# Kernel tuning notes

Hardware: AMD Instinct MI355X
Metric: run time of the kernel (lower is better)

## Reference

```python
import jax, jax.numpy as jnp
import numpy as np

V = 50257  # vocab
D = 256    # embedding size
H = 256    # hidden size
E = 64     # pre-allocated entity slots (replaces dynamic torch.cat growth)
T = 2048   # sequence length


def setup_inputs() -> dict:
    key = jax.random.key(0)
    ks = jax.random.split(key, 16)

    def n(k, shape, s=0.02):
        return (jax.random.normal(k, shape) * s).astype(jnp.float32)

    r_emb = n(ks[0], (2, H))
    # Equation 7: entity slot init = r_emb[1] + sigma*noise, L2-normalized per row
    noise = jax.random.normal(ks[1], (E, H)).astype(jnp.float32)
    u = r_emb[1][None, :] + 0.01 * noise
    entities_init = u / jnp.linalg.norm(u, axis=-1, keepdims=True)

    return dict(
        tokens=jax.random.randint(ks[2], (T,), 0, V),
        entity_ids=jax.random.randint(ks[3], (T,), 0, E),
        emb=n(ks[4], (V, D)),
        W_ih=n(ks[5], (4 * H, D)),
        W_hh=n(ks[6], (4 * H, H)),
        b_ih=jnp.zeros((4 * H,), jnp.float32),
        b_hh=jnp.zeros((4 * H,), jnp.float32),
        out_W=n(ks[7], (V, H)),
        out_b=jnp.zeros((V,), jnp.float32),
        r_emb=r_emb,
        Wr_W=n(ks[8], (1, H, H)), Wr_b=jnp.zeros((1,), jnp.float32),
        Wlen_W=n(ks[9], (25, 2 * H)), Wlen_b=jnp.zeros((25,), jnp.float32),
        Went_W=n(ks[10], (1, H, H)), Went_b=jnp.zeros((1,), jnp.float32),
        wdist_W=n(ks[11], (1, 1)), wdist_b=jnp.zeros((1,), jnp.float32),
        Wdelta_W=n(ks[12], (1, H, H)), Wdelta_b=jnp.zeros((1,), jnp.float32),
        We_W=n(ks[13], (H, H)), We_b=jnp.zeros((H,), jnp.float32),
        entities_init=entities_init,
        dist_init=jnp.zeros((E, 1), jnp.float32),
    )


def _forward(tokens, entity_ids, emb, W_ih, W_hh, b_ih, b_hh, out_W, out_b,
             r_emb, Wr_W, Wr_b, Wlen_W, Wlen_b, Went_W, Went_b,
             wdist_W, wdist_b, Wdelta_W, Wdelta_b, We_W, We_b,
             entities_init, dist_init):
    def step(carry, inp):
        h, c, ents, dists, t = carry
        tok, eid = inp
        # single-step LSTM (torch gate order i, f, g, o)
        x = emb[tok]
        gates = W_ih @ x + b_ih + W_hh @ h + b_hh
        i_, f_, g_, o_ = jnp.split(gates, 4)
        c = jax.nn.sigmoid(f_) * c + jax.nn.sigmoid(i_) * jnp.tanh(g_)
        h = jax.nn.sigmoid(o_) * jnp.tanh(c)
        # Equation 3: pred_r = Bilinear(r_emb, h)  -> [2]
        pred_r = r_emb @ (Wr_W[0] @ h) + Wr_b[0]
        # Equation 4: entity scores with distance feature  -> [E]
        dist = dists[:, 0] - t                                    # dist_features - t
        h_aug = h[None, :] + (dist[:, None] * wdist_W[0, 0] + wdist_b[0])  # [E,H]
        pred_e = jnp.sum((ents @ Went_W[0]) * h_aug, axis=-1) + Went_b[0]
        # current entity read (gather)
        e_cur = ents[eid]
        # Equation 5: length head  -> [25]
        pred_l = Wlen_W @ jnp.concatenate([h, e_cur]) + Wlen_b
        # next-word logits  -> [V]
        pred_x = out_W @ (h + We_W @ e_cur + We_b) + out_b
        # Equation 8: entity update + scatter
        delta = jax.nn.sigmoid(e_cur @ (Wdelta_W[0] @ h) + Wdelta_b[0])
        u = delta * e_cur + (1.0 - delta) * h
        u = u / jnp.linalg.norm(u)
        ents = ents.at[eid].set(u)
        dists = dists.at[eid, 0].set(t)
        out = jnp.concatenate([pred_r, pred_e, pred_l, pred_x])  # [2+E+25+V]
        return (h, c, ents, dists, t + 1.0), out

    carry0 = (jnp.zeros((H,), jnp.float32), jnp.zeros((H,), jnp.float32),
              entities_init, dist_init, jnp.float32(0.0))
    _, outs = jax.lax.scan(step, carry0, (tokens, entity_ids))
    return outs  # [T, 2+E+25+V]


def reference(tokens, entity_ids, emb, W_ih, W_hh, b_ih, b_hh, out_W, out_b,
              r_emb, Wr_W, Wr_b, Wlen_W, Wlen_b, Went_W, Went_b,
              wdist_W, wdist_b, Wdelta_W, Wdelta_b, We_W, We_b,
              entities_init, dist_init):
    return _forward(tokens, entity_ids, emb, W_ih, W_hh, b_ih, b_hh, out_W, out_b,
                    r_emb, Wr_W, Wr_b, Wlen_W, Wlen_b, Went_W, Went_b,
                    wdist_W, wdist_b, Wdelta_W, Wdelta_b, We_W, We_b,
                    entities_init, dist_init)
```

## Files before the change

kernel.cpp:

```cpp
#include <hip/hip_runtime.h>
#include <cstdint>
#include <cstddef>

#define V_  50257
#define H_  256
#define E_  64
#define T_  2048
#define G4_ 1024
#define OSTRIDE 50348
#define CMROWS 820
#define PSTR 832
#define NGRP 16
#define RPB 52
#define NPREB 32
#define WSTR 257

typedef __attribute__((ext_vector_type(2))) _Float16 half2v;
typedef __attribute__((ext_vector_type(8))) short short8v;
typedef __attribute__((ext_vector_type(4))) float floatx4;

__device__ __forceinline__ float fdot2u(unsigned a, unsigned b, float acc){
  return __builtin_amdgcn_fdot2(__builtin_bit_cast(half2v, a),
                                __builtin_bit_cast(half2v, b), acc, false);
}
__device__ __forceinline__ unsigned packh2(float a, float b){
  half2v h; h.x = (_Float16)a; h.y = (_Float16)b;
  return __builtin_bit_cast(unsigned, h);
}
__device__ __forceinline__ unsigned short f2bf(float f){
  unsigned u = __builtin_bit_cast(unsigned, f);
  u += 0x7fffu + ((u >> 16) & 1u);
  return (unsigned short)(u >> 16);
}
__device__ __forceinline__ float sigm(float x){
  return __builtin_amdgcn_rcpf(1.0f + __expf(-x));
}
__device__ __forceinline__ float tanh_f(float x){
  float e = __expf(2.0f * x);
  return (e - 1.0f) * __builtin_amdgcn_rcpf(e + 1.0f);
}
__device__ __forceinline__ float dot4(uint4 w, uint4 h, float acc){
  acc = fdot2u(w.x, h.x, acc); acc = fdot2u(w.y, h.y, acc);
  acc = fdot2u(w.z, h.z, acc); acc = fdot2u(w.w, h.w, acc);
  return acc;
}

__device__ __forceinline__ int ldi_rlx(int* p){
  return __hip_atomic_load(p, __ATOMIC_RELAXED, __HIP_MEMORY_SCOPE_AGENT);
}
__device__ __forceinline__ float ldf_rlx(const float* p){
  return __hip_atomic_load(p, __ATOMIC_RELAXED, __HIP_MEMORY_SCOPE_AGENT);
}
__device__ __forceinline__ void stf_rlx(float* p, float v){
  __hip_atomic_store(p, v, __ATOMIC_RELAXED, __HIP_MEMORY_SCOPE_AGENT);
}
__device__ __forceinline__ void flag_add(int* p){
  (void)__hip_atomic_fetch_add(p, 1, __ATOMIC_RELAXED, __HIP_MEMORY_SCOPE_AGENT);
}

__global__ void k_prep(const float* __restrict__ out_W, const float* __restrict__ W_ih,
                       const float* __restrict__ W_hh,
                       unsigned short* __restrict__ OWB, float* __restrict__ WT,
                       unsigned* __restrict__ WP){
  const long n0 = (long)V_ * H_;
  const long n1 = (long)G4_ * H_;
  const long n2 = 32l * G4_;
  const long total = n0 + n1 + n2;
  for (long id = (long)blockIdx.x * blockDim.x + threadIdx.x; id < total;
       id += (long)gridDim.x * blockDim.x){
    if (id < n0){
      OWB[id] = f2bf(out_W[id]);
    } else if (id < n0 + n1){
      long i = id - n0;
      int r = (int)(i & 1023), k = (int)(i >> 10);
      WT[i] = W_ih[r * H_ + k];
    } else {
      long i = id - n0 - n1;
      int t = (int)(i & 1023), j4 = (int)(i >> 10);
      int r0 = t >> 2, s = t & 3;
      #pragma unroll
      for (int d = 0; d < 4; ++d){
        int j = j4 * 4 + d;
        int ri = j >> 5, c = j & 31;
        int grow = ri * H_ + r0;
        int k0 = s * 64 + c * 2;
        WP[(j4 * 1024 + t) * 4 + d] = packh2(W_hh[grow * H_ + k0],
                                             W_hh[grow * H_ + k0 + 1]);
      }
    }
  }
}

__global__ void k_cm(const float* __restrict__ Wdelta, const float* __restrict__ Went,
                     const float* __restrict__ We, const float* __restrict__ r_emb,
                     const float* __restrict__ Wr, const float* __restrict__ Wlen,
                     float* __restrict__ CMR){
  const int total = CMROWS * H_;
  for (int id = blockIdx.x * blockDim.x + threadIdx.x; id < total;
       id += gridDim.x * blockDim.x){
    int r = id >> 8, k = id & 255;
    float v;
    if (r < 256)      v = Wdelta[r * H_ + k];
    else if (r < 512) v = Went[k * H_ + (r - 256)];
    else if (r < 768) v = We[(r - 512) * H_ + k];
    else if (r < 770){
      int i = r - 768; float acc = 0.f;
      for (int m = 0; m < H_; ++m) acc += r_emb[i * H_ + m] * Wr[m * H_ + k];
      v = acc;
    }
    else if (r < 795) v = Wlen[(r - 770) * 2 * H_ + k];
    else              v = Wlen[(r - 795) * 2 * H_ + H_ + k];
    CMR[r * H_ + k] = v;
  }
}

__global__ void k_init(const float* __restrict__ E0, const float* __restrict__ Went,
                       const float* __restrict__ We, const float* __restrict__ Wlen,
                       float* __restrict__ GI, float* __restrict__ MST,
                       float* __restrict__ LST, float* __restrict__ ENTS){
  const int nG = E_ * H_, nM = E_ * H_, nL = E_ * 32, nC = E_ * H_;
  const int total = nG + nM + nL + nC;
  for (int id = blockIdx.x * blockDim.x + threadIdx.x; id < total;
       id += gridDim.x * blockDim.x){
    if (id < nG){
      int j = id >> 8, i = id & 255; float a = 0.f;
      for (int k = 0; k < H_; ++k) a += E0[j * H_ + k] * Went[k * H_ + i];
      GI[id] = a;
    } else if (id < nG + nM){
      int x = id - nG; int j = x >> 8, i = x & 255; float a = 0.f;
      for (int k = 0; k < H_; ++k) a += E0[j * H_ + k] * We[i * H_ + k];
      MST[x] = a;
    } else if (id < nG + nM + nL){
      int x = id - nG - nM; int j = x >> 5, i = x & 31; float a = 0.f;
      if (i < 25)
        for (int k = 0; k < H_; ++k) a += E0[j * H_ + k] * Wlen[i * 2 * H_ + H_ + k];
      LST[x] = a;
    } else {
      int x = id - nG - nM - nL;
      ENTS[x] = E0[x];
    }
  }
}

__global__ __launch_bounds__(1024) void k_a(const int* __restrict__ tokens,
                                            const float* __restrict__ emb,
                                            const float* __restrict__ WT,
                                            const float* __restrict__ b_ih,
                                            const float* __restrict__ b_hh,
                                            float* __restrict__ A4){
  __shared__ __align__(16) float xs[H_][8];
  const int t0 = blockIdx.x * 8;
  const int tid = threadIdx.x;
  for (int id = tid; id < 8 * H_; id += 1024){
    int k = id >> 3, tl = id & 7;
    xs[k][tl] = emb[(size_t)tokens[t0 + tl] * H_ + k];
  }
  __syncthreads();
  const int r = tid;
  const float base = b_ih[r] + b_hh[r];
  float acc[8];
  #pragma unroll
  for (int i = 0; i < 8; ++i) acc[i] = base;
  for (int k = 0; k < H_; ++k){
    float w = WT[k * G4_ + r];
    floatx4 x0 = *(const floatx4*)&xs[k][0];
    floatx4 x1 = *(const floatx4*)&xs[k][4];
    acc[0] += w * x0.x; acc[1] += w * x0.y; acc[2] += w * x0.z; acc[3] += w * x0.w;
    acc[4] += w * x1.x; acc[5] += w * x1.y; acc[6] += w * x1.z; acc[7] += w * x1.w;
  }
  const int r0 = r & 255, g = r >> 8;
  #pragma unroll
  for (int tl = 0; tl < 8; ++tl)
    A4[(((t0 + tl) * H_ + r0) << 2) + g] = acc[tl];
}

struct LstmS { unsigned hsh[4 * 36]; uint4 olds[7 * 512]; };
struct PreS  { float wrow[RPB * WSTR]; float hbuf[H_]; };
struct EntS  {
  unsigned Gsh[E_ * 132];
  unsigned hsh2[2][128];
  float Hld[2][H_], Dld[2][H_], Wld[2][H_], Vld[2][H_];
  float EXs[2][64];
  float Ssh[E_], DSH[E_];
  float red[8][2];
  float sc[4];
};
union PipeS { LstmS l; PreS p; EntS e; };

__global__ __launch_bounds__(512, 1) void k_pipe(
    const uint4* __restrict__ WP4, const floatx4* __restrict__ A4,
    float* Hws, const float* __restrict__ CMR, float* PRE,
    const int* __restrict__ ids, const float* __restrict__ GI,
    const float* __restrict__ dist_init, const float* __restrict__ We_b,
    const float* __restrict__ Wlen_b, const float* __restrict__ wdW,
    const float* __restrict__ wdB, const float* __restrict__ WdeltaB,
    const float* __restrict__ WentB, const float* __restrict__ WrB,
    float* __restrict__ ENTS, float* __restrict__ MST, float* __restrict__ LST,
    unsigned short* __restrict__ Zb, float* __restrict__ out,
    int* prog_h, int* pre_done)
{
  __shared__ PipeS sm;
  const int tid = threadIdx.x;
  const int bid = blockIdx.x;

  if (bid == 0){
    unsigned* hsh = sm.l.hsh;
    uint4* olds = sm.l.olds;
    const int r0 = tid >> 1, s2 = tid & 1;
    const int tA = r0 * 4 + 2 * s2;
    const int tB = tA + 1;
    const int sA = 2 * s2;

    uint4 wA[32], wB[16];
    #pragma unroll
    for (int j4 = 0; j4 < 32; ++j4) wA[j4] = WP4[j4 * 1024 + tA];
    #pragma unroll
    for (int j4 = 0; j4 < 16; ++j4) wB[j4] = WP4[j4 * 1024 + tB];
    #pragma unroll
    for (int j4 = 24; j4 < 31; ++j4) olds[(j4 - 24) * 512 + tid] = WP4[j4 * 1024 + tB];
    if (tid < 144) hsh[tid] = 0u;

    const uint4* gsrc = &WP4[16 * 1024 + tB];
    uint4 g_cur = gsrc[0];
    float c = 0.0f;
    floatx4 a_cur = A4[r0];
    floatx4 a_nxt = a_cur;
    __syncthreads();

    for (int t = 0; t < T_; ++t){
      if (t + 1 < T_) a_nxt = A4[(t + 1) * H_ + r0];
      uint4 o_strm = gsrc[15 * 1024];
      float acc0 = a_cur.x * 0.5f, acc1 = a_cur.y * 0.5f;
      float acc2 = a_cur.z * 0.5f, acc3 = a_cur.w * 0.5f;
      #pragma unroll
      for (int cc = 0; cc < 8; ++cc){
        uint4 g_nxt = gsrc[((cc < 7) ? (cc + 1) : 0) * 1024];
        uint4 hA = *(const uint4*)&hsh[sA * 36 + cc * 4];
        uint4 hB = *(const uint4*)&hsh[sA * 36 + 36 + cc * 4];
        acc0 = dot4(wA[cc],      hA, acc0);
        acc1 = dot4(wA[8 + cc],  hA, acc1);
        acc2 = dot4(wA[16 + cc], hA, acc2);
        acc3 = dot4(wA[24 + cc], hA, acc3);
        acc0 = dot4(wB[cc],      hB, acc0);
        acc1 = dot4(wB[8 + cc],  hB, acc1);
        acc2 = dot4(g_cur,       hB, acc2);
        uint4 xo = (cc < 7) ? olds[cc * 512 + tid] : o_strm;
        acc3 = dot4(xo,          hB, acc3);
        g_cur = g_nxt;
      }
      acc0 += __shfl_xor(acc0, 1);
      acc1 += __shfl_xor(acc1, 1);
      acc2 += __shfl_xor(acc2, 1);
      acc3 += __shfl_xor(acc3, 1);
      float ci = sigm(acc0), cf = sigm(acc1), cg = tanh_f(acc2), co = sigm(acc3);
      c = cf * c + ci * cg;
      float hn = co * tanh_f(c);
      __syncthreads();
      if (s2 == 0){
        ((_Float16*)hsh)[(((r0 >> 6) * 36) + ((r0 >> 1) & 31)) * 2 + (r0 & 1)] = (_Float16)hn;
        stf_rlx(&Hws[t * H_ + r0], hn);
      }
      __syncthreads();
      if (tid == 0) flag_add(prog_h);
      a_cur = a_nxt;
    }
  } else if (bid <= NPREB){
    float* wrow = sm.p.wrow;
    float* hbuf = sm.p.hbuf;
    const int w9 = bid - 1;
    const int grp = w9 & (NGRP - 1), ph = w9 >> 4;
    const int rbase = grp * RPB;
    const int nrows = (rbase + RPB <= CMROWS) ? RPB : (CMROWS - rbase);
    for (int id = tid; id < nrows * H_; id += 512){
      int lr = id >> 8, k = id & 255;
      wrow[lr * WSTR + k] = CMR[(size_t)rbase * H_ + id];
    }
    __syncthreads();
    for (int t = ph; t < T_; t += 2){
      if (tid == 0){
        while (ldi_rlx(prog_h) < t + 1) __builtin_amdgcn_s_sleep(8);
      }
      __syncthreads();
      if (tid < H_) hbuf[tid] = ldf_rlx(&Hws[t * H_ + tid]);
      __syncthreads();
      if (tid < nrows){
        const float* wr = &wrow[tid * WSTR];
        float a = 0.f;
        #pragma unroll 8
        for (int k = 0; k < H_; ++k) a += wr[k] * hbuf[k];
        stf_rlx(&PRE[(size_t)t * PSTR + rbase + tid], a);
      }
      __syncthreads();
      if (tid == 0) flag_add(&pre_done[t]);
    }
  } else {
    EntS& E = sm.e;
    unsigned* Gsh = E.Gsh;
    auto& hsh2 = E.hsh2;
    auto& Hld = E.Hld; auto& Dld = E.Dld; auto& Wld = E.Wld; auto& Vld = E.Vld;
    auto& EXs = E.EXs;
    float* Ssh = E.Ssh; float* DSH = E.DSH;
    auto& red = E.red; float* sc = E.sc;

    for (int id = tid; id < E_ * 128; id += 512){
      int j = id >> 7, cx = id & 127;
      Gsh[j * 132 + cx] = packh2(GI[j * H_ + 2 * cx], GI[j * H_ + 2 * cx + 1]);
    }
    if (tid < E_){
      float ssum = 0.f;
      for (int k = 0; k < H_; ++k) ssum += GI[tid * H_ + k];
      Ssh[tid] = ssum;
      DSH[tid] = dist_init[tid];
    }
    const float wd = wdW[0], wdb = wdB[0], bdel = WdeltaB[0];
    const float wentb = WentB[0], wrb = WrB[0];
    int eid = ids[0];
    int eidn = ids[1];
    float e_k = 0.f, m_k = 0.f, web = 0.f;
    float l_i = 0.f, wlb = 0.f;
    if (tid == 0){
      while (ldi_rlx(&pre_done[0]) < NGRP) __builtin_amdgcn_s_sleep(2);
    }
    __syncthreads();
    if (tid < H_){
      e_k = ENTS[eid * H_ + tid];
      m_k = MST[eid * H_ + tid];
      web = We_b[tid];
      float h0 = ldf_rlx(&Hws[tid]);
      Hld[0][tid] = h0;
      ((_Float16*)&hsh2[0][0])[tid] = (_Float16)h0;
      Dld[0][tid] = ldf_rlx(&PRE[tid]);
      Wld[0][tid] = ldf_rlx(&PRE[256 + tid]);
      Vld[0][tid] = ldf_rlx(&PRE[512 + tid]);
    }
    if (tid < 25){ l_i = LST[eid * 32 + tid]; wlb = Wlen_b[tid]; }
    if (tid >= 256 && tid < 308) EXs[0][tid - 256] = ldf_rlx(&PRE[768 + (tid - 256)]);
    int dv = NGRP;
    if (T_ > 1) dv = ldi_rlx(&pre_done[1]);
    __syncthreads();

    const int jrow = tid >> 3, sl = tid & 7;
    const int wave = tid >> 6;

    for (int t = 0; t < T_; ++t){
      const int par = t & 1;
      float Hn = 0.f, Dn = 0.f, Wn = 0.f, Vn = 0.f, EXn = 0.f;
      if (t + 1 < T_){
        if (tid < 320 && dv < NGRP){
          while (ldi_rlx(&pre_done[t + 1]) < NGRP) __builtin_amdgcn_s_sleep(2);
        }
        if (tid < H_){
          Hn = ldf_rlx(&Hws[(t + 1) * H_ + tid]);
          float* p = &PRE[(size_t)(t + 1) * PSTR];
          Dn = ldf_rlx(&p[tid]); Wn = ldf_rlx(&p[256 + tid]); Vn = ldf_rlx(&p[512 + tid]);
        } else if (tid < 308){
          EXn = ldf_rlx(&PRE[(size_t)(t + 1) * PSTR + 768 + (tid - 256)]);
        }
        if (tid < 320)
          dv = (t + 2 < T_) ? ldi_rlx(&pre_done[t + 2]) : NGRP;
      }
      const int eid2 = ids[(t + 2 < T_) ? (t + 2) : (T_ - 1)];
      const bool swr = (eidn != eid);
      float e2 = 0.f, m2 = 0.f, l2 = 0.f;
      if (swr){
        if (tid < H_){ e2 = ENTS[eidn * H_ + tid]; m2 = MST[eidn * H_ + tid]; }
        if (tid < 25)  l2 = LST[eidn * 32 + tid];
      }
      float pe = 0.f;
      {
        const unsigned* gp = &Gsh[jrow * 132 + sl * 16];
        const unsigned* hp = &hsh2[par][sl * 16];
        uint4 g0 = *(const uint4*)&gp[0];
        uint4 g1 = *(const uint4*)&gp[4];
        uint4 g2 = *(const uint4*)&gp[8];
        uint4 g3 = *(const uint4*)&gp[12];
        uint4 h0 = *(const uint4*)&hp[0];
        uint4 h1 = *(const uint4*)&hp[4];
        uint4 h2 = *(const uint4*)&hp[8];
        uint4 h3 = *(const uint4*)&hp[12];
        pe = dot4(g0, h0, pe); pe = dot4(g1, h1, pe);
        pe = dot4(g2, h2, pe); pe = dot4(g3, h3, pe);
        pe += __shfl_xor(pe, 1); pe += __shfl_xor(pe, 2); pe += __shfl_xor(pe, 4);
      }
      if (sl == 0){
        float dist = DSH[jrow] - (float)t;
        out[(size_t)t * OSTRIDE + 2 + jrow] = pe + (dist * wd + wdb) * Ssh[jrow] + wentb;
      }
      if (tid < H_){
        float pd = e_k * Dld[par][tid];
        float pw = Wld[par][tid];
        #pragma unroll
        for (int m = 1; m < 64; m <<= 1){ pd += __shfl_xor(pd, m); pw += __shfl_xor(pw, m); }
        if ((tid & 63) == 0){ red[wave][0] = pd; red[wave][1] = pw; }
      }
      __syncthreads();
      if (tid == 0){
        float sd = red[0][0] + red[1][0] + red[2][0] + red[3][0];
        float swt = red[0][1] + red[1][1] + red[2][1] + red[3][1];
        sc[0] = sigm(sd + bdel);
        sc[1] = swt;
      }
      __syncthreads();
      const float del = sc[0];
      float u = 0.f;
      if (tid < H_){
        u = del * e_k + (1.0f - del) * Hld[par][tid];
        float pu = u * u;
        #pragma unroll
        for (int m = 1; m < 64; m <<= 1) pu += __shfl_xor(pu, m);
        if ((tid & 63) == 0) red[wave][0] = pu;
      }
      __syncthreads();
      if (tid == 0)
        sc[2] = __builtin_amdgcn_rsqf(red[0][0] + red[1][0] + red[2][0] + red[3][0]);
      __syncthreads();
      const float rn = sc[2];
      float un = 0.f, mn = 0.f;
      if (tid < H_){
        un = u * rn;
        ENTS[eid * H_ + tid] = un;
        mn = (del * m_k + (1.0f - del) * Vld[par][tid]) * rn;
        MST[eid * H_ + tid] = mn;
        float z = Hld[par][tid] + m_k + web;
        Zb[(size_t)t * H_ + tid] = f2bf(z);
      }
      if (tid < 128){
        unsigned gp2 = Gsh[eid * 132 + tid];
        half2v g = __builtin_bit_cast(half2v, gp2);
        float gl = (del * (float)g.x + (1.0f - del) * Wld[par][2 * tid    ]) * rn;
        float gh = (del * (float)g.y + (1.0f - del) * Wld[par][2 * tid + 1]) * rn;
        Gsh[eid * 132 + tid] = packh2(gl, gh);
      }
      float ln = 0.f;
      if (tid < 25){
        out[(size_t)t * OSTRIDE + 66 + tid] = EXs[par][2 + tid] + l_i + wlb;
        ln = (del * l_i + (1.0f - del) * EXs[par][27 + tid]) * rn;
        LST[eid * 32 + tid] = ln;
      }
      if (tid < 2) out[(size_t)t * OSTRIDE + tid] = EXs[par][tid] + wrb;
      if (tid == 0){
        Ssh[eid] = (del * Ssh[eid] + (1.0f - del) * sc[1]) * rn;
        DSH[eid] = (float)t;
      }
      if (t + 1 < T_){
        if (tid < H_){
          Hld[1 - par][tid] = Hn; Dld[1 - par][tid] = Dn;
          Wld[1 - par][tid] = Wn; Vld[1 - par][tid] = Vn;
          ((_Float16*)&hsh2[1 - par][0])[tid] = (_Float16)Hn;
        } else if (tid < 308){
          EXs[1 - par][tid - 256] = EXn;
        }
      }
      if (tid < H_){ e_k = swr ? e2 : un; m_k = swr ? m2 : mn; }
      if (tid < 25)  l_i = swr ? l2 : ln;
      eid = eidn; eidn = eid2;
      __syncthreads();
    }
  }
}

__global__ __launch_bounds__(256) void k_gemm(const unsigned short* __restrict__ OWB,
                                              const unsigned short* __restrict__ Zb,
                                              const float* __restrict__ out_b,
                                              float* __restrict__ out){
  __shared__ __align__(16) unsigned short Ash[128 * 72];
  __shared__ __align__(16) unsigned short Bsh[128 * 72];
  const int t0 = blockIdx.x * 128;
  const int v0 = blockIdx.y * 128;
  const int tid = threadIdx.x;
  const int lane = tid & 63, w = tid >> 6;
  const int mb = (w & 1) * 64, nb = (w >> 1) * 64;
  const int q = lane >> 4, fr = lane & 15;
  floatx4 acc[4][4];
  #pragma unroll
  for (int a = 0; a < 4; ++a)
    #pragma unroll
    for (int b = 0; b < 4; ++b) acc[a][b] = (floatx4){0.f, 0.f, 0.f, 0.f};
  for (int kt = 0; kt < 4; ++kt){
    if (kt) __syncthreads();
    #pragma unroll
    for (int it = 0; it < 4; ++it){
      int task = it * 256 + tid;
      int r = task >> 3, c8 = task & 7;
      int gk = kt * 64 + c8 * 8;
      uint4 av;
      if (v0 + r < V_) av = *(const uint4*)&OWB[(size_t)(v0 + r) * H_ + gk];
      else { av.x = 0; av.y = 0; av.z = 0; av.w = 0; }
      *(uint4*)&Ash[r * 72 + c8 * 8] = av;
      uint4 bv = *(const uint4*)&Zb[(size_t)(t0 + r) * H_ + gk];
      *(uint4*)&Bsh[r * 72 + c8 * 8] = bv;
    }
    __syncthreads();
    #pragma unroll
    for (int ks = 0; ks < 2; ++ks){
      short8v af[4], bf[4];
      #pragma unroll
      for (int mi = 0; mi < 4; ++mi)
        af[mi] = *(const short8v*)&Ash[(mb + mi * 16 + fr) * 72 + ks * 32 + q * 8];
      #pragma unroll
      for (int ni = 0; ni < 4; ++ni)
        bf[ni] = *(const short8v*)&Bsh[(nb + ni * 16 + fr) * 72 + ks * 32 + q * 8];
      #pragma unroll
      for (int mi = 0; mi < 4; ++mi)
        #pragma unroll
        for (int ni = 0; ni < 4; ++ni)
          acc[mi][ni] = __builtin_amdgcn_mfma_f32_16x16x32_bf16(af[mi], bf[ni],
                                                                acc[mi][ni], 0, 0, 0);
    }
  }
  #pragma unroll
  for (int mi = 0; mi < 4; ++mi){
    #pragma unroll
    for (int ni = 0; ni < 4; ++ni){
      int tt = t0 + nb + ni * 16 + fr;
      int vv = v0 + mb + mi * 16 + q * 4;
      float* op = out + (size_t)tt * OSTRIDE + 91 + vv;
      #pragma unroll
      for (int r2 = 0; r2 < 4; ++r2){
        int v = vv + r2;
        if (v < V_) op[r2] = acc[mi][ni][r2] + out_b[v];
      }
    }
  }
}

extern "C" void kernel_launch(void* const* d_in, const int* in_sizes, int n_in,
                              void* d_out, int out_size, void* d_ws, size_t ws_size,
                              hipStream_t stream){
  (void)in_sizes; (void)n_in; (void)out_size; (void)ws_size;
  const int*   tokens  = (const int*)d_in[0];
  const int*   eids    = (const int*)d_in[1];
  const float* emb     = (const float*)d_in[2];
  const float* W_ih    = (const float*)d_in[3];
  const float* W_hh    = (const float*)d_in[4];
  const float* b_ih    = (const float*)d_in[5];
  const float* b_hh    = (const float*)d_in[6];
  const float* out_W   = (const float*)d_in[7];
  const float* out_b   = (const float*)d_in[8];
  const float* r_emb   = (const float*)d_in[9];
  const float* Wr_W    = (const float*)d_in[10];
  const float* Wr_b    = (const float*)d_in[11];
  const float* Wlen_W  = (const float*)d_in[12];
  const float* Wlen_b  = (const float*)d_in[13];
  const float* Went_W  = (const float*)d_in[14];
  const float* Went_b  = (const float*)d_in[15];
  const float* wdist_W = (const float*)d_in[16];
  const float* wdist_b = (const float*)d_in[17];
  const float* Wdelta_W= (const float*)d_in[18];
  const float* Wdelta_b= (const float*)d_in[19];
  const float* We_W    = (const float*)d_in[20];
  const float* We_b    = (const float*)d_in[21];
  const float* E0      = (const float*)d_in[22];
  const float* dist0   = (const float*)d_in[23];
  float* out = (float*)d_out;

  char* ws = (char*)d_ws;
  size_t off = 0;
  auto alloc = [&](size_t bytes) -> void* {
    void* p = ws + off;
    off += (bytes + 255) & ~(size_t)255;
    return p;
  };
  float* WT    = (float*)alloc(sizeof(float) * H_ * G4_);
  float* A4    = (float*)alloc(sizeof(float) * (size_t)T_ * H_ * 4);
  unsigned* WP = (unsigned*)alloc(sizeof(unsigned) * 32 * 1024 * 4);
  float* Hws   = (float*)alloc(sizeof(float) * (size_t)T_ * H_);
  float* CMR   = (float*)alloc(sizeof(float) * CMROWS * H_);
  float* PRE   = (float*)alloc(sizeof(float) * (size_t)T_ * PSTR);
  float* ENTS  = (float*)alloc(sizeof(float) * E_ * H_);
  float* MST   = (float*)alloc(sizeof(float) * E_ * H_);
  float* LST   = (float*)alloc(sizeof(float) * E_ * 32);
  float* GI    = (float*)alloc(sizeof(float) * E_ * H_);
  unsigned short* Zb  = (unsigned short*)alloc(sizeof(short) * (size_t)T_ * H_);
  unsigned short* OWB = (unsigned short*)alloc(sizeof(short) * (size_t)V_ * H_);
  int* pre_done = (int*)alloc(sizeof(int) * (T_ + 64));
  int* prog_h   = pre_done + T_;

  hipMemsetAsync(pre_done, 0, sizeof(int) * (T_ + 64), stream);
  hipLaunchKernelGGL(k_prep, dim3(4096), dim3(256), 0, stream,
                     out_W, W_ih, W_hh, OWB, WT, WP);
  hipLaunchKernelGGL(k_cm, dim3(512), dim3(256), 0, stream,
                     Wdelta_W, Went_W, We_W, r_emb, Wr_W, Wlen_W, CMR);
  hipLaunchKernelGGL(k_init, dim3(256), dim3(256), 0, stream,
                     E0, Went_W, We_W, Wlen_W, GI, MST, LST, ENTS);
  hipLaunchKernelGGL(k_a, dim3(T_ / 8), dim3(1024), 0, stream,
                     tokens, emb, WT, b_ih, b_hh, A4);
  hipLaunchKernelGGL(k_pipe, dim3(2 + NPREB), dim3(512), 0, stream,
                     (const uint4*)WP, (const floatx4*)A4, Hws, CMR, PRE,
                     eids, GI, dist0, We_b, Wlen_b,
                     wdist_W, wdist_b, Wdelta_b, Went_b, Wr_b,
                     ENTS, MST, LST, Zb, out, prog_h, pre_done);
  hipLaunchKernelGGL(k_gemm, dim3(16, 393), dim3(256), 0, stream,
                     OWB, Zb, out_b, out);
}
```

Measured before the change: 4.444 ms.

## Fuse vocab GEMM into persistent pipeline kernel, overlapping with sequential entity recurrence

Moves the output-projection GEMM into the persistent pipeline kernel as 222 extra blocks. Each block waits on an entity-progress counter and computes 128x128 tiles as soon as the matching Zb rows are written, so the large GEMM overlaps the serial recurrence instead of running after it. The change also merges the k_cm, k_init and memset work into k_prep, and removes two barriers per step in the entity loop by having every thread do the reductions. In exchange, all blocks must be co-resident because of the spin-waits, which risks deadlock or contention with the latency-critical recurrence blocks, and half the threads in each GEMM block sit idle during the MFMA phase.

```diff
diff --git a/kernel.cpp b/kernel.cpp
--- a/kernel.cpp
+++ b/kernel.cpp
@@ -14,6 +14,9 @@
 #define RPB 52
 #define NPREB 32
 #define WSTR 257
+#define NGEMB 222
+#define NTILT 16
+#define NTILV 393
 
 typedef __attribute__((ext_vector_type(2))) _Float16 half2v;
 typedef __attribute__((ext_vector_type(8))) short short8v;
@@ -59,13 +62,23 @@
 }
 
 __global__ void k_prep(const float* __restrict__ out_W, const float* __restrict__ W_ih,
-                       const float* __restrict__ W_hh,
+                       const float* __restrict__ W_hh, const float* __restrict__ Wdelta,
+                       const float* __restrict__ Went, const float* __restrict__ We,
+                       const float* __restrict__ r_emb, const float* __restrict__ Wr,
+                       const float* __restrict__ Wlen, const float* __restrict__ E0,
                        unsigned short* __restrict__ OWB, float* __restrict__ WT,
-                       unsigned* __restrict__ WP){
+                       unsigned* __restrict__ WP, float* __restrict__ CMR,
+                       float* __restrict__ GI, float* __restrict__ MST,
+                       float* __restrict__ LST, float* __restrict__ ENTS,
+                       int* __restrict__ FLG){
   const long n0 = (long)V_ * H_;
   const long n1 = (long)G4_ * H_;
   const long n2 = 32l * G4_;
-  const long total = n0 + n1 + n2;
+  const long n3 = (long)CMROWS * H_;
+  const long nG = E_ * H_, nM = E_ * H_, nL = E_ * 32, nC = E_ * H_;
+  const long n4 = nG + nM + nL + nC;
+  const long n5 = T_ + 64;
+  const long total = n0 + n1 + n2 + n3 + n4 + n5;
   for (long id = (long)blockIdx.x * blockDim.x + threadIdx.x; id < total;
        id += (long)gridDim.x * blockDim.x){
     if (id < n0){
@@ -74,7 +87,7 @@
       long i = id - n0;
       int r = (int)(i & 1023), k = (int)(i >> 10);
       WT[i] = W_ih[r * H_ + k];
-    } else {
+    } else if (id < n0 + n1 + n2){
       long i = id - n0 - n1;
       int t = (int)(i & 1023), j4 = (int)(i >> 10);
       int r0 = t >> 2, s = t & 3;
@@ -87,57 +100,42 @@
         WP[(j4 * 1024 + t) * 4 + d] = packh2(W_hh[grow * H_ + k0],
                                              W_hh[grow * H_ + k0 + 1]);
       }
-    }
-  }
-}
-
-__global__ void k_cm(const float* __restrict__ Wdelta, const float* __restrict__ Went,
-                     const float* __restrict__ We, const float* __restrict__ r_emb,
-                     const float* __restrict__ Wr, const float* __restrict__ Wlen,
-                     float* __restrict__ CMR){
-  const int total = CMROWS * H_;
-  for (int id = blockIdx.x * blockDim.x + threadIdx.x; id < total;
-       id += gridDim.x * blockDim.x){
-    int r = id >> 8, k = id & 255;
-    float v;
-    if (r < 256)      v = Wdelta[r * H_ + k];
-    else if (r < 512) v = Went[k * H_ + (r - 256)];
-    else if (r < 768) v = We[(r - 512) * H_ + k];
-    else if (r < 770){
-      int i = r - 768; float acc = 0.f;
-      for (int m = 0; m < H_; ++m) acc += r_emb[i * H_ + m] * Wr[m * H_ + k];
-      v = acc;
-    }
-    else if (r < 795) v = Wlen[(r - 770) * 2 * H_ + k];
-    else              v = Wlen[(r - 795) * 2 * H_ + H_ + k];
-    CMR[r * H_ + k] = v;
-  }
-}
-
-__global__ void k_init(const float* __restrict__ E0, const float* __restrict__ Went,
-                       const float* __restrict__ We, const float* __restrict__ Wlen,
-                       float* __restrict__ GI, float* __restrict__ MST,
-                       float* __restrict__ LST, float* __restrict__ ENTS){
-  const int nG = E_ * H_, nM = E_ * H_, nL = E_ * 32, nC = E_ * H_;
-  const int total = nG + nM + nL + nC;
-  for (int id = blockIdx.x * blockDim.x + threadIdx.x; id < total;
-       id += gridDim.x * blockDim.x){
-    if (id < nG){
-      int j = id >> 8, i = id & 255; float a = 0.f;
-      for (int k = 0; k < H_; ++k) a += E0[j * H_ + k] * Went[k * H_ + i];
-      GI[id] = a;
-    } else if (id < nG + nM){
-      int x = id - nG; int j = x >> 8, i = x & 255; float a = 0.f;
-      for (int k = 0; k < H_; ++k) a += E0[j * H_ + k] * We[i * H_ + k];
-      MST[x] = a;
-    } else if (id < nG + nM + nL){
-      int x = id - nG - nM; int j = x >> 5, i = x & 31; float a = 0.f;
-      if (i < 25)
-        for (int k = 0; k < H_; ++k) a += E0[j * H_ + k] * Wlen[i * 2 * H_ + H_ + k];
-      LST[x] = a;
+    } else if (id < n0 + n1 + n2 + n3){
+      long i = id - n0 - n1 - n2;
+      int r = (int)(i >> 8), k = (int)(i & 255);
+      float v;
+      if (r < 256)      v = Wdelta[r * H_ + k];
+      else if (r < 512) v = Went[k * H_ + (r - 256)];
+      else if (r < 768) v = We[(r - 512) * H_ + k];
+      else if (r < 770){
+        int ii = r - 768; float acc = 0.f;
+        for (int m = 0; m < H_; ++m) acc += r_emb[ii * H_ + m] * Wr[m * H_ + k];
+        v = acc;
+      }
+      else if (r < 795) v = Wlen[(r - 770) * 2 * H_ + k];
+      else              v = Wlen[(r - 795) * 2 * H_ + H_ + k];
+      CMR[i] = v;
+    } else if (id < n0 + n1 + n2 + n3 + n4){
+      long x = id - n0 - n1 - n2 - n3;
+      if (x < nG){
+        int j = (int)(x >> 8), i = (int)(x & 255); float a = 0.f;
+        for (int k = 0; k < H_; ++k) a += E0[j * H_ + k] * Went[k * H_ + i];
+        GI[x] = a;
+      } else if (x < nG + nM){
+        long y = x - nG; int j = (int)(y >> 8), i = (int)(y & 255); float a = 0.f;
+        for (int k = 0; k < H_; ++k) a += E0[j * H_ + k] * We[i * H_ + k];
+        MST[y] = a;
+      } else if (x < nG + nM + nL){
+        long y = x - nG - nM; int j = (int)(y >> 5), i = (int)(y & 31); float a = 0.f;
+        if (i < 25)
+          for (int k = 0; k < H_; ++k) a += E0[j * H_ + k] * Wlen[i * 2 * H_ + H_ + k];
+        LST[y] = a;
+      } else {
+        long y = x - nG - nM - nL;
+        ENTS[y] = E0[y];
+      }
     } else {
-      int x = id - nG - nM - nL;
-      ENTS[x] = E0[x];
+      FLG[id - (n0 + n1 + n2 + n3 + n4)] = 0;
     }
   }
 }
@@ -182,12 +180,13 @@
   float Hld[2][H_], Dld[2][H_], Wld[2][H_], Vld[2][H_];
   float EXs[2][64];
   float Ssh[E_], DSH[E_];
-  float red[8][2];
-  float sc[4];
+  float red[4][4];
 };
-union PipeS { LstmS l; PreS p; EntS e; };
-
-__global__ __launch_bounds__(512, 1) void k_pipe(
+struct GemmS { unsigned short Ash[128 * 72]; unsigned short Bsh[128 * 72]; };
+union __align__(16) PipeS { LstmS l; PreS p; EntS e; GemmS g; };
+
+__global__ __launch_bounds__(512) __attribute__((amdgpu_waves_per_eu(2, 2)))
+void k_pipe(
     const uint4* __restrict__ WP4, const floatx4* __restrict__ A4,
     float* Hws, const float* __restrict__ CMR, float* PRE,
     const int* __restrict__ ids, const float* __restrict__ GI,
@@ -196,8 +195,9 @@
     const float* __restrict__ wdB, const float* __restrict__ WdeltaB,
     const float* __restrict__ WentB, const float* __restrict__ WrB,
     float* __restrict__ ENTS, float* __restrict__ MST, float* __restrict__ LST,
-    unsigned short* __restrict__ Zb, float* __restrict__ out,
-    int* prog_h, int* pre_done)
+    unsigned short* Zb, const unsigned short* __restrict__ OWB,
+    const float* __restrict__ out_b, float* __restrict__ out,
+    int* prog_h, int* pre_done, int* ent_prog)
 {
   __shared__ PipeS sm;
   const int tid = threadIdx.x;
@@ -293,14 +293,14 @@
       __syncthreads();
       if (tid == 0) flag_add(&pre_done[t]);
     }
-  } else {
+  } else if (bid == NPREB + 1){
     EntS& E = sm.e;
     unsigned* Gsh = E.Gsh;
     auto& hsh2 = E.hsh2;
     auto& Hld = E.Hld; auto& Dld = E.Dld; auto& Wld = E.Wld; auto& Vld = E.Vld;
     auto& EXs = E.EXs;
     float* Ssh = E.Ssh; float* DSH = E.DSH;
-    auto& red = E.red; float* sc = E.sc;
+    auto& red = E.red;
 
     for (int id = tid; id < E_ * 128; id += 512){
       int j = id >> 7, cx = id & 127;
@@ -344,6 +344,11 @@
 
     for (int t = 0; t < T_; ++t){
       const int par = t & 1;
+      if (tid < H_){
+        float z = Hld[par][tid] + m_k + web;
+        __hip_atomic_store(&Zb[(size_t)t * H_ + tid], f2bf(z),
+                           __ATOMIC_RELAXED, __HIP_MEMORY_SCOPE_AGENT);
+      }
       float Hn = 0.f, Dn = 0.f, Wn = 0.f, Vn = 0.f, EXn = 0.f;
       if (t + 1 < T_){
         if (tid < 320 && dv < NGRP){
@@ -394,35 +399,27 @@
         if ((tid & 63) == 0){ red[wave][0] = pd; red[wave][1] = pw; }
       }
       __syncthreads();
-      if (tid == 0){
-        float sd = red[0][0] + red[1][0] + red[2][0] + red[3][0];
-        float swt = red[0][1] + red[1][1] + red[2][1] + red[3][1];
-        sc[0] = sigm(sd + bdel);
-        sc[1] = swt;
-      }
-      __syncthreads();
-      const float del = sc[0];
+      const float sd  = red[0][0] + red[1][0] + red[2][0] + red[3][0];
+      const float swt = red[0][1] + red[1][1] + red[2][1] + red[3][1];
+      const float del = sigm(sd + bdel);
       float u = 0.f;
       if (tid < H_){
         u = del * e_k + (1.0f - del) * Hld[par][tid];
         float pu = u * u;
         #pragma unroll
         for (int m = 1; m < 64; m <<= 1) pu += __shfl_xor(pu, m);
-        if ((tid & 63) == 0) red[wave][0] = pu;
-      }
-      __syncthreads();
-      if (tid == 0)
-        sc[2] = __builtin_amdgcn_rsqf(red[0][0] + red[1][0] + red[2][0] + red[3][0]);
-      __syncthreads();
-      const float rn = sc[2];
+        if ((tid & 63) == 0) red[wave][2] = pu;
+      }
+      __syncthreads();
+      const float rn = __builtin_amdgcn_rsqf(red[0][2] + red[1][2] +
+                                             red[2][2] + red[3][2]);
+      if (tid == 0) flag_add(ent_prog);
       float un = 0.f, mn = 0.f;
       if (tid < H_){
         un = u * rn;
         ENTS[eid * H_ + tid] = un;
         mn = (del * m_k + (1.0f - del) * Vld[par][tid]) * rn;
         MST[eid * H_ + tid] = mn;
-        float z = Hld[par][tid] + m_k + web;
-        Zb[(size_t)t * H_ + tid] = f2bf(z);
       }
       if (tid < 128){
         unsigned gp2 = Gsh[eid * 132 + tid];
@@ -439,7 +436,7 @@
       }
       if (tid < 2) out[(size_t)t * OSTRIDE + tid] = EXs[par][tid] + wrb;
       if (tid == 0){
-        Ssh[eid] = (del * Ssh[eid] + (1.0f - del) * sc[1]) * rn;
+        Ssh[eid] = (del * Ssh[eid] + (1.0f - del) * swt) * rn;
         DSH[eid] = (float)t;
       }
       if (t + 1 < T_){
@@ -456,70 +453,84 @@
       eid = eidn; eidn = eid2;
       __syncthreads();
     }
-  }
-}
-
-__global__ __launch_bounds__(256) void k_gemm(const unsigned short* __restrict__ OWB,
-                                              const unsigned short* __restrict__ Zb,
-                                              const float* __restrict__ out_b,
-                                              float* __restrict__ out){
-  __shared__ __align__(16) unsigned short Ash[128 * 72];
-  __shared__ __align__(16) unsigned short Bsh[128 * 72];
-  const int t0 = blockIdx.x * 128;
-  const int v0 = blockIdx.y * 128;
-  const int tid = threadIdx.x;
-  const int lane = tid & 63, w = tid >> 6;
-  const int mb = (w & 1) * 64, nb = (w >> 1) * 64;
-  const int q = lane >> 4, fr = lane & 15;
-  floatx4 acc[4][4];
-  #pragma unroll
-  for (int a = 0; a < 4; ++a)
-    #pragma unroll
-    for (int b = 0; b < 4; ++b) acc[a][b] = (floatx4){0.f, 0.f, 0.f, 0.f};
-  for (int kt = 0; kt < 4; ++kt){
-    if (kt) __syncthreads();
-    #pragma unroll
-    for (int it = 0; it < 4; ++it){
-      int task = it * 256 + tid;
-      int r = task >> 3, c8 = task & 7;
-      int gk = kt * 64 + c8 * 8;
-      uint4 av;
-      if (v0 + r < V_) av = *(const uint4*)&OWB[(size_t)(v0 + r) * H_ + gk];
-      else { av.x = 0; av.y = 0; av.z = 0; av.w = 0; }
-      *(uint4*)&Ash[r * 72 + c8 * 8] = av;
-      uint4 bv = *(const uint4*)&Zb[(size_t)(t0 + r) * H_ + gk];
-      *(uint4*)&Bsh[r * 72 + c8 * 8] = bv;
-    }
-    __syncthreads();
-    #pragma unroll
-    for (int ks = 0; ks < 2; ++ks){
-      short8v af[4], bf[4];
+  } else {
+    unsigned short* Ash = sm.g.Ash;
+    unsigned short* Bsh = sm.g.Bsh;
+    const int gid = bid - (NPREB + 2);
+    const int lane = tid & 63, w = tid >> 6;
+    const int mb = (w & 1) * 64, nb = ((w >> 1) & 1) * 64;
+    const int q = lane >> 4, fr = lane & 15;
+    for (int task = gid; task < NTILT * NTILV; task += NGEMB){
+      const int tt = task / NTILV, vv = task - tt * NTILV;
+      const int t0 = tt * 128, v0 = vv * 128;
+      if (tid == 0){
+        while (ldi_rlx(ent_prog) < t0 + 128) __builtin_amdgcn_s_sleep(16);
+      }
+      __syncthreads();
+      floatx4 acc[4][4];
       #pragma unroll
-      for (int mi = 0; mi < 4; ++mi)
-        af[mi] = *(const short8v*)&Ash[(mb + mi * 16 + fr) * 72 + ks * 32 + q * 8];
-      #pragma unroll
-      for (int ni = 0; ni < 4; ++ni)
-        bf[ni] = *(const short8v*)&Bsh[(nb + ni * 16 + fr) * 72 + ks * 32 + q * 8];
-      #pragma unroll
-      for (int mi = 0; mi < 4; ++mi)
+      for (int a = 0; a < 4; ++a)
         #pragma unroll
-        for (int ni = 0; ni < 4; ++ni)
-          acc[mi][ni] = __builtin_amdgcn_mfma_f32_16x16x32_bf16(af[mi], bf[ni],
-                                                                acc[mi][ni], 0, 0, 0);
-    }
-  }
-  #pragma unroll
-  for (int mi = 0; mi < 4; ++mi){
-    #pragma unroll
-    for (int ni = 0; ni < 4; ++ni){
-      int tt = t0 + nb + ni * 16 + fr;
-      int vv = v0 + mb + mi * 16 + q * 4;
-      float* op = out + (size_t)tt * OSTRIDE + 91 + vv;
-      #pragma unroll
-      for (int r2 = 0; r2 < 4; ++r2){
-        int v = vv + r2;
-        if (v < V_) op[r2] = acc[mi][ni][r2] + out_b[v];
-      }
+        for (int b = 0; b < 4; ++b) acc[a][b] = (floatx4){0.f, 0.f, 0.f, 0.f};
+      for (int kt = 0; kt < 4; ++kt){
+        if (kt) __syncthreads();
+        #pragma unroll
+        for (int it = 0; it < 2; ++it){
+          int id2 = it * 512 + tid;
+          int r = id2 >> 3, c8 = id2 & 7;
+          int gk = kt * 64 + c8 * 8;
+          uint4 av;
+          if (v0 + r < V_) av = *(const uint4*)&OWB[(size_t)(v0 + r) * H_ + gk];
+          else { av.x = 0; av.y = 0; av.z = 0; av.w = 0; }
+          *(uint4*)&Ash[r * 72 + c8 * 8] = av;
+          const unsigned long long* zp =
+              (const unsigned long long*)&Zb[(size_t)(t0 + r) * H_ + gk];
+          unsigned long long z0 = __hip_atomic_load(zp, __ATOMIC_RELAXED,
+                                                    __HIP_MEMORY_SCOPE_AGENT);
+          unsigned long long z1 = __hip_atomic_load(zp + 1, __ATOMIC_RELAXED,
+                                                    __HIP_MEMORY_SCOPE_AGENT);
+          uint4 bv;
+          bv.x = (unsigned)z0; bv.y = (unsigned)(z0 >> 32);
+          bv.z = (unsigned)z1; bv.w = (unsigned)(z1 >> 32);
+          *(uint4*)&Bsh[r * 72 + c8 * 8] = bv;
+        }
+        __syncthreads();
+        if (tid < 256){
+          #pragma unroll
+          for (int ks = 0; ks < 2; ++ks){
+            short8v af[4], bf[4];
+            #pragma unroll
+            for (int mi = 0; mi < 4; ++mi)
+              af[mi] = *(const short8v*)&Ash[(mb + mi * 16 + fr) * 72 + ks * 32 + q * 8];
+            #pragma unroll
+            for (int ni = 0; ni < 4; ++ni)
+              bf[ni] = *(const short8v*)&Bsh[(nb + ni * 16 + fr) * 72 + ks * 32 + q * 8];
+            #pragma unroll
+            for (int mi = 0; mi < 4; ++mi)
+              #pragma unroll
+              for (int ni = 0; ni < 4; ++ni)
+                acc[mi][ni] = __builtin_amdgcn_mfma_f32_16x16x32_bf16(af[mi], bf[ni],
+                                                                      acc[mi][ni], 0, 0, 0);
+          }
+        }
+      }
+      if (tid < 256){
+        #pragma unroll
+        for (int mi = 0; mi < 4; ++mi){
+          #pragma unroll
+          for (int ni = 0; ni < 4; ++ni){
+            int tt2 = t0 + nb + ni * 16 + fr;
+            int vv2 = v0 + mb + mi * 16 + q * 4;
+            float* op = out + (size_t)tt2 * OSTRIDE + 91 + vv2;
+            #pragma unroll
+            for (int r2 = 0; r2 < 4; ++r2){
+              int v = vv2 + r2;
+              if (v < V_) op[r2] = acc[mi][ni][r2] + out_b[v];
+            }
+          }
+        }
+      }
+      __syncthreads();
     }
   }
 }
@@ -575,21 +586,17 @@
   unsigned short* OWB = (unsigned short*)alloc(sizeof(short) * (size_t)V_ * H_);
   int* pre_done = (int*)alloc(sizeof(int) * (T_ + 64));
   int* prog_h   = pre_done + T_;
-
-  hipMemsetAsync(pre_done, 0, sizeof(int) * (T_ + 64), stream);
+  int* ent_prog = pre_done + T_ + 1;
+
   hipLaunchKernelGGL(k_prep, dim3(4096), dim3(256), 0, stream,
-                     out_W, W_ih, W_hh, OWB, WT, WP);
-  hipLaunchKernelGGL(k_cm, dim3(512), dim3(256), 0, stream,
-                     Wdelta_W, Went_W, We_W, r_emb, Wr_W, Wlen_W, CMR);
-  hipLaunchKernelGGL(k_init, dim3(256), dim3(256), 0, stream,
-                     E0, Went_W, We_W, Wlen_W, GI, MST, LST, ENTS);
+                     out_W, W_ih, W_hh, Wdelta_W, Went_W, We_W, r_emb, Wr_W,
+                     Wlen_W, E0, OWB, WT, WP, CMR, GI, MST, LST, ENTS, pre_done);
   hipLaunchKernelGGL(k_a, dim3(T_ / 8), dim3(1024), 0, stream,
                      tokens, emb, WT, b_ih, b_hh, A4);
-  hipLaunchKernelGGL(k_pipe, dim3(2 + NPREB), dim3(512), 0, stream,
+  hipLaunchKernelGGL(k_pipe, dim3(2 + NPREB + NGEMB), dim3(512), 0, stream,
                      (const uint4*)WP, (const floatx4*)A4, Hws, CMR, PRE,
                      eids, GI, dist0, We_b, Wlen_b,
                      wdist_W, wdist_b, Wdelta_b, Went_b, Wr_b,
-                     ENTS, MST, LST, Zb, out, prog_h, pre_done);
-  hipLaunchKernelGGL(k_gemm, dim3(16, 393), dim3(256), 0, stream,
-                     OWB, Zb, out_b, out);
-}
+                     ENTS, MST, LST, Zb, OWB, out_b, out,
+                     prog_h, pre_done, ent_prog);
+}
```

New measurement: 4.638 ms. 1.04x slower.
